# Performance work log

Hardware: AMD Instinct MI355X
Metric: run time of the kernel (lower is better)

Reference implementation:

```python
import jax, jax.numpy as jnp
import numpy as np

IN_F = 128
OUT_F = 128
N_NODES = 50000
N_EDGES = 800000


def setup_inputs() -> dict:
    key = jax.random.key(0)
    k_x, k_e, k_w, k_b = jax.random.split(key, 4)
    x = jax.random.normal(k_x, (N_NODES, IN_F), dtype=jnp.float32)
    edge_index = jax.random.randint(k_e, (2, N_EDGES), 0, N_NODES, dtype=jnp.int64)
    # linear params (torch nn.Linear: y = x @ W.T + b)
    bound = 1.0 / np.sqrt(IN_F)
    W = jax.random.uniform(k_w, (OUT_F, IN_F), minval=-bound, maxval=bound, dtype=jnp.float32)
    b = jax.random.uniform(k_b, (OUT_F,), minval=-bound, maxval=bound, dtype=jnp.float32)
    return {"x": x, "edge_index": edge_index, "n_nodes": N_NODES, "W": W, "b": b}


def reference(x, edge_index, n_nodes, W, b):
    row, col = edge_index[0], edge_index[1]
    # gather source features and segment-sum into destination nodes
    agg = jax.ops.segment_sum(x[row], col, num_segments=n_nodes)  # [N, in_f]
    # in-degree, clamped to 1 (bincount + clamp in torch)
    deg = jax.ops.segment_sum(jnp.ones_like(col, dtype=jnp.float32), col, num_segments=n_nodes)
    deg = jnp.maximum(deg, 1.0)
    h = agg / deg[:, None]
    return h @ W.T + b
```

## Files before the change

### kernel.cpp

```cpp
#include <hip/hip_runtime.h>

#define IN_F 128
#define OUT_F 128

typedef unsigned int uint32;
typedef unsigned short ushort16;
using short8 = __attribute__((ext_vector_type(8))) short;
using f32x4  = __attribute__((ext_vector_type(4))) float;

__device__ __forceinline__ uint32 f2bf(float f) {
    const uint32 u = __float_as_uint(f);
    return (u + 0x7FFFu + ((u >> 16) & 1u)) >> 16;
}
__device__ __forceinline__ uint32 pack_bf2(float lo, float hi) {
    return f2bf(lo) | (f2bf(hi) << 16);
}

__global__ __launch_bounds__(256) void k_cvt(
    const float* __restrict__ x, const float* __restrict__ W,
    uint32* __restrict__ xb, uint32* __restrict__ wb, int nx4, int nw4)
{
    const int i4 = blockIdx.x * 256 + threadIdx.x;
    if (i4 < nx4) {
        const float4 v = reinterpret_cast<const float4*>(x)[i4];
        uint2 st;
        st.x = pack_bf2(v.x, v.y);
        st.y = pack_bf2(v.z, v.w);
        reinterpret_cast<uint2*>(xb)[i4] = st;
    } else if (i4 - nx4 < nw4) {
        const int j4 = i4 - nx4;
        const float4 v = reinterpret_cast<const float4*>(W)[j4];
        uint2 st;
        st.x = pack_bf2(v.x, v.y);
        st.y = pack_bf2(v.z, v.w);
        reinterpret_cast<uint2*>(wb)[j4] = st;
    }
}

__global__ __launch_bounds__(256) void k_hist(
    const int* __restrict__ ei, int* __restrict__ deg_i, int nEdges)
{
    int e = blockIdx.x * blockDim.x + threadIdx.x;
    if (e < nEdges) {
        atomicAdd(&deg_i[ei[nEdges + e]], 1);
    }
}

__global__ __launch_bounds__(256) void k_scan_a(
    const int* __restrict__ deg_i, int* __restrict__ escan,
    int* __restrict__ bsum, int n)
{
    __shared__ int sh[256];
    const int t = threadIdx.x;
    const int i = blockIdx.x * 256 + t;
    int v = (i < n) ? deg_i[i] : 0;
    sh[t] = v;
    __syncthreads();
    for (int ofs = 1; ofs < 256; ofs <<= 1) {
        int u = (t >= ofs) ? sh[t - ofs] : 0;
        __syncthreads();
        sh[t] += u;
        __syncthreads();
    }
    if (i < n) escan[i] = sh[t] - v;
    if (t == 255) bsum[blockIdx.x] = sh[255];
}

__global__ __launch_bounds__(256) void k_scan_b(
    const int* __restrict__ bsum, int* __restrict__ bbase, int nb)
{
    __shared__ int sh[256];
    const int t = threadIdx.x;
    int v = (t < nb) ? bsum[t] : 0;
    sh[t] = v;
    __syncthreads();
    for (int ofs = 1; ofs < 256; ofs <<= 1) {
        int u = (t >= ofs) ? sh[t - ofs] : 0;
        __syncthreads();
        sh[t] += u;
        __syncthreads();
    }
    if (t < nb) bbase[t] = sh[t] - v;
}

__global__ __launch_bounds__(256) void k_scan_c(
    const int* __restrict__ escan, const int* __restrict__ bbase,
    int* __restrict__ off, int* __restrict__ cursor, int n)
{
    const int i = blockIdx.x * 256 + threadIdx.x;
    if (i < n) {
        const int o = escan[i] + bbase[blockIdx.x];
        off[i] = o;
        cursor[i] = o;
    }
}

__global__ __launch_bounds__(256) void k_scatter_ids(
    const int* __restrict__ ei, int* __restrict__ cursor,
    int* __restrict__ perm, int nEdges)
{
    int e = blockIdx.x * blockDim.x + threadIdx.x;
    if (e < nEdges) {
        const int src = ei[e];
        const int dst = ei[nEdges + e];
        const int pos = atomicAdd(&cursor[dst], 1);
        perm[pos] = src;
    }
}

__global__ __launch_bounds__(256) void k_gather(
    const uint32* __restrict__ xb2,
    const int* __restrict__ perm,
    const int* __restrict__ off,
    const int* __restrict__ deg_i,
    uint32* __restrict__ hb2,
    int nNodes)
{
    const int node = (blockIdx.x << 2) + (threadIdx.x >> 6);
    const int lane = threadIdx.x & 63;
    if (node >= nNodes) return;

    const int s = off[node];
    const int d = deg_i[node];

    float ax = 0.0f, ay = 0.0f;
    int i = 0;
    for (; i + 4 <= d; i += 4) {
        const uint32 u0 = xb2[(size_t)perm[s + i + 0] * 64 + lane];
        const uint32 u1 = xb2[(size_t)perm[s + i + 1] * 64 + lane];
        const uint32 u2 = xb2[(size_t)perm[s + i + 2] * 64 + lane];
        const uint32 u3 = xb2[(size_t)perm[s + i + 3] * 64 + lane];
        ax += __uint_as_float(u0 << 16);
        ay += __uint_as_float(u0 & 0xFFFF0000u);
        ax += __uint_as_float(u1 << 16);
        ay += __uint_as_float(u1 & 0xFFFF0000u);
        ax += __uint_as_float(u2 << 16);
        ay += __uint_as_float(u2 & 0xFFFF0000u);
        ax += __uint_as_float(u3 << 16);
        ay += __uint_as_float(u3 & 0xFFFF0000u);
    }
    for (; i < d; ++i) {
        const uint32 u = xb2[(size_t)perm[s + i] * 64 + lane];
        ax += __uint_as_float(u << 16);
        ay += __uint_as_float(u & 0xFFFF0000u);
    }

    const float inv = 1.0f / (float)(d > 0 ? d : 1);
    hb2[(size_t)node * 64 + lane] = pack_bf2(ax * inv, ay * inv);
}

__global__ __launch_bounds__(256) void k_mm(
    const ushort16* __restrict__ hbf,
    const ushort16* __restrict__ wbf,
    const float* __restrict__ bias,
    float* __restrict__ out, int nNodes)
{
    const int wave = threadIdx.x >> 6;
    const int lane = threadIdx.x & 63;
    const int m0 = blockIdx.x * 128 + wave * 32;
    const int lrow = lane & 15;
    const int kgrp = lane >> 4;

    short8 a[2][4];
#pragma unroll
    for (int mt = 0; mt < 2; ++mt) {
        int mrow = m0 + mt * 16 + lrow;
        if (mrow >= nNodes) mrow = nNodes - 1;
        const ushort16* hrow = hbf + (size_t)mrow * IN_F;
#pragma unroll
        for (int kt = 0; kt < 4; ++kt) {
            a[mt][kt] = *reinterpret_cast<const short8*>(hrow + kt * 32 + kgrp * 8);
        }
    }

#pragma unroll
    for (int nt = 0; nt < 8; ++nt) {
        const int n0 = nt * 16;
        const ushort16* wrow = wbf + (size_t)(n0 + lrow) * IN_F;
        const float bv = bias[n0 + lrow];

        f32x4 acc0 = {bv, bv, bv, bv};
        f32x4 acc1 = {bv, bv, bv, bv};
#pragma unroll
        for (int kt = 0; kt < 4; ++kt) {
            const short8 b = *reinterpret_cast<const short8*>(wrow + kt * 32 + kgrp * 8);
            acc0 = __builtin_amdgcn_mfma_f32_16x16x32_bf16(a[0][kt], b, acc0, 0, 0, 0);
            acc1 = __builtin_amdgcn_mfma_f32_16x16x32_bf16(a[1][kt], b, acc1, 0, 0, 0);
        }
#pragma unroll
        for (int r = 0; r < 4; ++r) {
            const int row0 = m0 + kgrp * 4 + r;
            const int row1 = m0 + 16 + kgrp * 4 + r;
            if (row0 < nNodes) out[(size_t)row0 * OUT_F + n0 + lrow] = acc0[r];
            if (row1 < nNodes) out[(size_t)row1 * OUT_F + n0 + lrow] = acc1[r];
        }
    }
}

extern "C" void kernel_launch(void* const* d_in, const int* in_sizes, int n_in,
                              void* d_out, int out_size, void* d_ws, size_t ws_size,
                              hipStream_t stream)
{
    const float* x   = (const float*)d_in[0];
    const int*   ei  = (const int*)d_in[1];
    const float* W   = (const float*)d_in[3];
    const float* b   = (const float*)d_in[4];
    float*       out = (float*)d_out;

    const int nNodes = in_sizes[0] / IN_F;
    const int nEdges = in_sizes[1] / 2;
    const int nb = (nNodes + 255) / 256;

    int* deg_i  = (int*)d_ws;
    int* off    = deg_i + nNodes;
    int* cursor = off + nNodes;
    int* escan  = cursor + nNodes;
    int* bsum   = escan + nNodes;
    int* bbase  = bsum + nb;
    int* perm   = bbase + nb;
    ushort16* hbf = (ushort16*)(perm + nEdges);
    ushort16* wbf = hbf + (size_t)nNodes * IN_F;

    uint32* xb = (uint32*)d_out;

    (void)hipMemsetAsync(deg_i, 0, (size_t)nNodes * sizeof(int), stream);

    const int nx4 = (nNodes * IN_F) / 4;
    const int nw4 = (OUT_F * IN_F) / 4;
    k_cvt<<<(nx4 + nw4 + 255) / 256, 256, 0, stream>>>(x, W, xb, (uint32*)wbf,
                                                       nx4, nw4);

    const int eb = (nEdges + 255) / 256;
    k_hist<<<eb, 256, 0, stream>>>(ei, deg_i, nEdges);

    k_scan_a<<<nb, 256, 0, stream>>>(deg_i, escan, bsum, nNodes);
    k_scan_b<<<1, 256, 0, stream>>>(bsum, bbase, nb);
    k_scan_c<<<nb, 256, 0, stream>>>(escan, bbase, off, cursor, nNodes);

    k_scatter_ids<<<eb, 256, 0, stream>>>(ei, cursor, perm, nEdges);

    const int gb = (nNodes + 3) / 4;
    k_gather<<<gb, 256, 0, stream>>>(xb, perm, off, deg_i,
                                     (uint32*)hbf, nNodes);

    const int mb = (nNodes + 127) / 128;
    k_mm<<<mb, 256, 0, stream>>>(hbf, wbf, b, out, nNodes);
}
```

Baseline: 164.2 us.

## Replace per-edge global atomic scatter with two-pass bucketed counting sort

The single scatter pass, which did one global atomic per edge on per-node cursors, becomes two passes. First, edges are binned into 128-node buckets with global atomics on per-bucket cursors, storing packed (local dst, src) words. Second, each block sorts its bucket into the CSR perm array using shared-memory atomics. The aim is more local writes and cheaper final atomics. The cost is an extra pass over the edges, heavy contention on the few bucket counters, and a 16-bit src encoding that only works for fewer than 65536 nodes.

```diff
diff --git a/kernel.cpp b/kernel.cpp
--- a/kernel.cpp
+++ b/kernel.cpp
@@ -2,6 +2,7 @@
 
 #define IN_F 128
 #define OUT_F 128
+#define BNODES 128
 
 typedef unsigned int uint32;
 typedef unsigned short ushort16;
@@ -85,25 +86,66 @@
 
 __global__ __launch_bounds__(256) void k_scan_c(
     const int* __restrict__ escan, const int* __restrict__ bbase,
-    int* __restrict__ off, int* __restrict__ cursor, int n)
+    int* __restrict__ off, int* __restrict__ bcurB, int n)
 {
     const int i = blockIdx.x * 256 + threadIdx.x;
     if (i < n) {
         const int o = escan[i] + bbase[blockIdx.x];
         off[i] = o;
-        cursor[i] = o;
-    }
-}
-
-__global__ __launch_bounds__(256) void k_scatter_ids(
-    const int* __restrict__ ei, int* __restrict__ cursor,
-    int* __restrict__ perm, int nEdges)
-{
-    int e = blockIdx.x * blockDim.x + threadIdx.x;
-    if (e < nEdges) {
-        const int src = ei[e];
-        const int dst = ei[nEdges + e];
-        const int pos = atomicAdd(&cursor[dst], 1);
+        if ((i & (BNODES - 1)) == 0) bcurB[i >> 7] = o;
+    }
+}
+
+__global__ __launch_bounds__(256) void k_bin(
+    const int* __restrict__ ei, int* __restrict__ bcurB,
+    uint32* __restrict__ ebuf, int nEdges)
+{
+    const int e0 = (blockIdx.x * 256 + threadIdx.x) * 4;
+    if (e0 + 4 <= nEdges) {
+        const int4 src4 = *reinterpret_cast<const int4*>(ei + e0);
+        const int4 dst4 = *reinterpret_cast<const int4*>(ei + nEdges + e0);
+        int pos;
+        pos = atomicAdd(&bcurB[dst4.x >> 7], 1);
+        ebuf[pos] = ((uint32)(dst4.x & (BNODES - 1)) << 16) | (uint32)src4.x;
+        pos = atomicAdd(&bcurB[dst4.y >> 7], 1);
+        ebuf[pos] = ((uint32)(dst4.y & (BNODES - 1)) << 16) | (uint32)src4.y;
+        pos = atomicAdd(&bcurB[dst4.z >> 7], 1);
+        ebuf[pos] = ((uint32)(dst4.z & (BNODES - 1)) << 16) | (uint32)src4.z;
+        pos = atomicAdd(&bcurB[dst4.w >> 7], 1);
+        ebuf[pos] = ((uint32)(dst4.w & (BNODES - 1)) << 16) | (uint32)src4.w;
+    } else {
+        for (int e = e0; e < nEdges; ++e) {
+            const int src = ei[e];
+            const int dst = ei[nEdges + e];
+            const int pos = atomicAdd(&bcurB[dst >> 7], 1);
+            ebuf[pos] = ((uint32)(dst & (BNODES - 1)) << 16) | (uint32)src;
+        }
+    }
+}
+
+__global__ __launch_bounds__(256) void k_sort(
+    const uint32* __restrict__ ebuf, const int* __restrict__ off,
+    int* __restrict__ perm, int nNodes, int nEdges, int nb)
+{
+    __shared__ int cur[BNODES];
+    const int b = blockIdx.x;
+    const int t = threadIdx.x;
+
+    const int node0 = b * BNODES;
+    if (t < BNODES) {
+        const int node = node0 + t;
+        cur[t] = (node < nNodes) ? off[node] : 0;
+    }
+    __syncthreads();
+
+    const int s = off[node0];
+    const int e = (b == nb - 1) ? nEdges : off[node0 + BNODES];
+
+    for (int i = s + t; i < e; i += 256) {
+        const uint32 u = ebuf[i];
+        const int ld  = (int)(u >> 16);
+        const int src = (int)(u & 0xFFFFu);
+        const int pos = atomicAdd(&cur[ld], 1);
         perm[pos] = src;
     }
 }
@@ -209,15 +251,17 @@
 
     const int nNodes = in_sizes[0] / IN_F;
     const int nEdges = in_sizes[1] / 2;
-    const int nb = (nNodes + 255) / 256;
-
-    int* deg_i  = (int*)d_ws;
-    int* off    = deg_i + nNodes;
-    int* cursor = off + nNodes;
-    int* escan  = cursor + nNodes;
-    int* bsum   = escan + nNodes;
-    int* bbase  = bsum + nb;
-    int* perm   = bbase + nb;
+    const int nb  = (nNodes + BNODES - 1) / BNODES;
+    const int nsb = (nNodes + 255) / 256;
+
+    int*    deg_i = (int*)d_ws;
+    int*    off   = deg_i + nNodes;
+    int*    escan = off + nNodes;
+    int*    bsum  = escan + nNodes;
+    int*    bbase = bsum + nsb;
+    int*    bcurB = bbase + nsb;
+    uint32* ebuf  = (uint32*)(bcurB + nb);
+    int*    perm  = (int*)(ebuf + nEdges);
     ushort16* hbf = (ushort16*)(perm + nEdges);
     ushort16* wbf = hbf + (size_t)nNodes * IN_F;
 
@@ -233,15 +277,17 @@
     const int eb = (nEdges + 255) / 256;
     k_hist<<<eb, 256, 0, stream>>>(ei, deg_i, nEdges);
 
-    k_scan_a<<<nb, 256, 0, stream>>>(deg_i, escan, bsum, nNodes);
-    k_scan_b<<<1, 256, 0, stream>>>(bsum, bbase, nb);
-    k_scan_c<<<nb, 256, 0, stream>>>(escan, bbase, off, cursor, nNodes);
-
-    k_scatter_ids<<<eb, 256, 0, stream>>>(ei, cursor, perm, nEdges);
+    k_scan_a<<<nsb, 256, 0, stream>>>(deg_i, escan, bsum, nNodes);
+    k_scan_b<<<1, 256, 0, stream>>>(bsum, bbase, nsb);
+    k_scan_c<<<nsb, 256, 0, stream>>>(escan, bbase, off, bcurB, nNodes);
+
+    const int bb = (nEdges / 4 + 255) / 256;
+    k_bin<<<bb, 256, 0, stream>>>(ei, bcurB, ebuf, nEdges);
+
+    k_sort<<<nb, 256, 0, stream>>>(ebuf, off, perm, nNodes, nEdges, nb);
 
     const int gb = (nNodes + 3) / 4;
-    k_gather<<<gb, 256, 0, stream>>>(xb, perm, off, deg_i,
-                                     (uint32*)hbf, nNodes);
+    k_gather<<<gb, 256, 0, stream>>>(xb, perm, off, deg_i, (uint32*)hbf, nNodes);
 
     const int mb = (nNodes + 127) / 128;
     k_mm<<<mb, 256, 0, stream>>>(hbf, wbf, b, out, nNodes);
```

After: 398.3 us. 142% more time.
